# Optimization experiments

Measured on AMD Instinct MI355X. Metric: run time of the kernel, lower is better.

Reference implementation:

```python
import jax, jax.numpy as jnp
import numpy as np

N_NODES = 50000
N_EDGES = 800000
H = 128   # hidden_dim
E = 64    # edge_dim
LN_EPS = 1e-5


def _layer_norm(x, g, b):
    m = jnp.mean(x, axis=-1, keepdims=True)
    v = jnp.mean(jnp.square(x - m), axis=-1, keepdims=True)
    return (x - m) * jax.lax.rsqrt(v + LN_EPS) * g + b


def _gelu(x):
    return jax.nn.gelu(x, approximate=False)  # torch default exact GELU


def setup_inputs() -> dict:
    key = jax.random.key(0)
    ks = jax.random.split(key, 24)

    def lin(k, fin, fout):
        kw, kb = jax.random.split(k)
        s = 1.0 / np.sqrt(fin)
        W = jax.random.uniform(kw, (fin, fout), jnp.float32, -s, s)
        b = jax.random.uniform(kb, (fout,), jnp.float32, -s, s)
        return W, b

    inp = {}
    inp["x"] = jax.random.normal(ks[0], (N_NODES, H), jnp.float32)
    inp["edge_emb"] = jax.random.normal(ks[1], (N_EDGES, E), jnp.float32)
    inp["time_weight"] = jax.random.uniform(ks[2], (N_EDGES, 1), jnp.float32)
    inp["message_node_scale"] = jax.random.uniform(ks[3], (N_NODES, 1), jnp.float32)
    inp["ln1_g"] = jnp.ones((H,), jnp.float32)
    inp["ln1_b"] = jnp.zeros((H,), jnp.float32)
    inp["ln2_g"] = jnp.ones((H,), jnp.float32)
    inp["ln2_b"] = jnp.zeros((H,), jnp.float32)
    inp["selfW"], inp["selfb"] = lin(ks[4], H, H)
    inp["msgW1"], inp["msgb1"] = lin(ks[5], H + E, H)
    inp["msgW2"], inp["msgb2"] = lin(ks[6], H, H)
    inp["gateW1"], inp["gateb1"] = lin(ks[7], 2 * H + E, H)
    inp["gateW2"], inp["gateb2"] = lin(ks[8], H, 1)
    inp["aggW"], inp["aggb"] = lin(ks[9], H, H)
    inp["ffnW1"], inp["ffnb1"] = lin(ks[10], H, 2 * H)
    inp["ffnW2"], inp["ffnb2"] = lin(ks[11], 2 * H, H)
    inp["edge_src"] = jax.random.randint(ks[12], (N_EDGES,), 0, N_NODES, jnp.int32)
    inp["edge_dst"] = jax.random.randint(ks[13], (N_EDGES,), 0, N_NODES, jnp.int32)
    return inp


def reference(x, edge_emb, time_weight, message_node_scale,
              ln1_g, ln1_b, ln2_g, ln2_b,
              selfW, selfb, msgW1, msgb1, msgW2, msgb2,
              gateW1, gateb1, gateW2, gateb2,
              aggW, aggb, ffnW1, ffnb1, ffnW2, ffnb2,
              edge_src, edge_dst):
    n_nodes = x.shape[0]
    n_edges = edge_dst.shape[0]

    h = _layer_norm(x, ln1_g, ln1_b)
    hs = h[edge_src]  # [NE, H]
    hd = h[edge_dst]  # [NE, H]

    msg = _gelu(jnp.concatenate([hs, edge_emb], -1) @ msgW1 + msgb1) @ msgW2 + msgb2
    gate = jax.nn.sigmoid(
        _gelu(jnp.concatenate([hd, hs, edge_emb], -1) @ gateW1 + gateb1) @ gateW2 + gateb2)
    edge_repr = gate * msg
    edge_repr = edge_repr * time_weight
    edge_scale = 0.5 * (message_node_scale[edge_src] + message_node_scale[edge_dst])
    edge_repr = edge_repr * edge_scale

    agg = jax.ops.segment_sum(edge_repr, edge_dst, num_segments=n_nodes)
    deg = jax.ops.segment_sum(jnp.ones((n_edges, 1), x.dtype), edge_dst,
                              num_segments=n_nodes)
    agg = agg / jnp.maximum(deg, 1.0)

    update = (h @ selfW + selfb) + (agg @ aggW + aggb)
    out = x + update  # residual; dropout is identity at inference

    h2 = _layer_norm(out, ln2_g, ln2_b)
    ffn_update = _gelu(h2 @ ffnW1 + ffnb1) @ ffnW2 + ffnb2
    out = out + ffn_update
    return (out, edge_repr)
```

## Files before the change

### kernel.cpp

```cpp
#include <hip/hip_runtime.h>


typedef __attribute__((ext_vector_type(8))) short short8;
typedef __attribute__((ext_vector_type(4))) float f32x4;

#define NN 50000
#define NEDGE 800000

#define MFMA(a, b, c) __builtin_amdgcn_mfma_f32_16x16x32_bf16(a, b, c, 0, 0, 0)

__device__ __forceinline__ unsigned short f2bf(float f) {
  unsigned int u = __float_as_uint(f);
  u += 0x7fffu + ((u >> 16) & 1u);
  return (unsigned short)(u >> 16);
}
__device__ __forceinline__ float bf2f(unsigned short u) {
  return __uint_as_float((unsigned int)u << 16);
}
__device__ __forceinline__ unsigned int cvtpk(float a, float b) {
  unsigned int d;
  asm("v_cvt_pk_bf16_f32 %0, %1, %2" : "=v"(d) : "v"(a), "v"(b));
  return d;
}
__device__ __forceinline__ unsigned short f2bf1(float a) {
  return (unsigned short)cvtpk(a, a);
}
__device__ __forceinline__ float geluf(float x) {
  const float t = x * fmaf(-0.1029437f, x * x, -2.3022211f);
  return x * __builtin_amdgcn_rcpf(1.0f + exp2f(t));
}
__device__ __forceinline__ short8 ld8(const unsigned short* p) {
  return *reinterpret_cast<const short8*>(p);
}
__device__ __forceinline__ int swz256(int row, int byteoff) {
  return row * 256 + (byteoff ^ ((row & 15) << 4));
}
__device__ __forceinline__ int swz128(int row, int byteoff) {
  return row * 128 + (byteoff ^ ((row & 7) << 4));
}

__device__ __forceinline__ void ln_frags(const float* __restrict__ rowp,
                                         const float* __restrict__ g,
                                         const float* __restrict__ b, int koff,
                                         short8 a[4]) {
  f32x4 v[8];
#pragma unroll
  for (int s = 0; s < 4; s++) {
    v[2 * s] = *reinterpret_cast<const f32x4*>(rowp + s * 32 + koff);
    v[2 * s + 1] = *reinterpret_cast<const f32x4*>(rowp + s * 32 + koff + 4);
  }
  float sm = 0.f;
#pragma unroll
  for (int i = 0; i < 8; i++) sm += v[i][0] + v[i][1] + v[i][2] + v[i][3];
  sm += __shfl_xor(sm, 16);
  sm += __shfl_xor(sm, 32);
  const float mean = sm * 0.0078125f;
  float sq = 0.f;
#pragma unroll
  for (int i = 0; i < 8; i++) {
#pragma unroll
    for (int t = 0; t < 4; t++) {
      const float d = v[i][t] - mean;
      sq += d * d;
    }
  }
  sq += __shfl_xor(sq, 16);
  sq += __shfl_xor(sq, 32);
  const float rs = rsqrtf(sq * 0.0078125f + 1e-5f);
#pragma unroll
  for (int s = 0; s < 4; s++) {
    const f32x4 glo = *reinterpret_cast<const f32x4*>(g + s * 32 + koff);
    const f32x4 ghi = *reinterpret_cast<const f32x4*>(g + s * 32 + koff + 4);
    const f32x4 blo = *reinterpret_cast<const f32x4*>(b + s * 32 + koff);
    const f32x4 bhi = *reinterpret_cast<const f32x4*>(b + s * 32 + koff + 4);
    float y[8];
#pragma unroll
    for (int t = 0; t < 4; t++) {
      y[t] = (v[2 * s][t] - mean) * rs * glo[t] + blo[t];
      y[4 + t] = (v[2 * s + 1][t] - mean) * rs * ghi[t] + bhi[t];
    }
    union { unsigned int u[4]; short8 s8; } pk;
    pk.u[0] = cvtpk(y[0], y[1]);
    pk.u[1] = cvtpk(y[2], y[3]);
    pk.u[2] = cvtpk(y[4], y[5]);
    pk.u[3] = cvtpk(y[6], y[7]);
    a[s] = pk.s8;
  }
}

__global__ __launch_bounds__(256) void prep_kernel(
    const float* __restrict__ selfW, const float* __restrict__ msgW1,
    const float* __restrict__ msgW2, const float* __restrict__ gateW1,
    const float* __restrict__ aggW, const float* __restrict__ ffnW1,
    const float* __restrict__ ffnW2, unsigned short* __restrict__ wts,
    int* __restrict__ cnt) {
  const int idx = blockIdx.x * 256 + threadIdx.x;
  if (idx <= NN) cnt[idx] = 0;
  if (idx < 16384) {
    int n = idx >> 7, k = idx & 127;
    wts[idx] = f2bf(selfW[k * 128 + n]);
  } else if (idx < 32768) {
    int l = idx - 16384, n = l >> 7, k = l & 127;
    wts[idx] = f2bf(aggW[k * 128 + n]);
  } else if (idx < 57344) {
    int l = idx - 32768, n = l / 192, k = l - n * 192;
    wts[idx] = f2bf(msgW1[k * 128 + n]);
  } else if (idx < 73728) {
    int l = idx - 57344, n = l >> 7, k = l & 127;
    wts[idx] = f2bf(msgW2[k * 128 + n]);
  } else if (idx < 114688) {
    int l = idx - 73728, n = l / 320, k = l - n * 320;
    wts[idx] = f2bf(gateW1[k * 128 + n]);
  } else if (idx < 147456) {
    int l = idx - 114688, n = l >> 7, k = l & 127;
    wts[idx] = f2bf(ffnW1[k * 256 + n]);
  } else if (idx < 180224) {
    int l = idx - 147456, n = l >> 8, k = l & 255;
    wts[idx] = f2bf(ffnW2[k * 128 + n]);
  }
}

__global__ __launch_bounds__(256) void node_pre_kernel(
    const float* __restrict__ x, const float* __restrict__ ln1g,
    const float* __restrict__ ln1b, const unsigned short* __restrict__ wts,
    unsigned short* __restrict__ pd, unsigned short* __restrict__ psm,
    float* __restrict__ aggf) {
  const int wid = threadIdx.x >> 6, lane = threadIdx.x & 63;
  const int q = lane >> 4, r16 = lane & 15, koff = q * 8;
  const int r0 = blockIdx.x * 64 + wid * 16;
  const int row = min(r0 + r16, NN - 1);
  {
    const int t = blockIdx.x * 256 + threadIdx.x;
    const f32x4 z = (f32x4){0.f, 0.f, 0.f, 0.f};
#pragma unroll
    for (int k = 0; k < 8; k++) {
      const int pos = t + k * 200192;
      if (pos < NN * 32) reinterpret_cast<f32x4*>(aggf)[pos] = z;
    }
  }
  const unsigned short* gateW1T = wts + 73728;
  const unsigned short* msgW1T = wts + 32768;
  short8 a[4];
  ln_frags(x + (size_t)row * 128, ln1g, ln1b, koff, a);
  f32x4 acc[3][8];
#pragma unroll
  for (int t = 0; t < 3; t++)
#pragma unroll
    for (int nt = 0; nt < 8; nt++) acc[t][nt] = (f32x4){0.f, 0.f, 0.f, 0.f};
#pragma unroll
  for (int s = 0; s < 4; s++) {
    const int k0 = s * 32 + koff;
#pragma unroll
    for (int nt = 0; nt < 8; nt++) {
      const int c = nt * 16 + r16;
      acc[0][nt] = MFMA(a[s], ld8(gateW1T + c * 320 + k0), acc[0][nt]);
      acc[1][nt] = MFMA(a[s], ld8(gateW1T + c * 320 + 128 + k0), acc[1][nt]);
      acc[2][nt] = MFMA(a[s], ld8(msgW1T + c * 192 + k0), acc[2][nt]);
    }
  }
#pragma unroll
  for (int j = 0; j < 4; j++) {
    const int gr = r0 + q * 4 + j;
    if (gr < NN) {
#pragma unroll
      for (int nt = 0; nt < 8; nt++) {
        const int c = nt * 16 + r16;
        pd[(size_t)gr * 128 + c] = f2bf(acc[0][nt][j]);
        psm[(size_t)gr * 256 + c] = f2bf(acc[1][nt][j]);
        psm[(size_t)gr * 256 + 128 + c] = f2bf(acc[2][nt][j]);
      }
    }
  }
}

__global__ __launch_bounds__(256) void count_kernel(
    const int* __restrict__ edst, int* __restrict__ cnt) {
  const int e = blockIdx.x * 256 + threadIdx.x;
  atomicAdd(&cnt[edst[e]], 1);
}

__global__ __launch_bounds__(256) void scan_sums_kernel(
    const int* __restrict__ cnt, int* __restrict__ bsum) {
  const int gi = blockIdx.x * 256 + threadIdx.x;
  int v = (gi < NN) ? cnt[gi] : 0;
#pragma unroll
  for (int m = 1; m < 64; m <<= 1) v += __shfl_xor(v, m);
  __shared__ int wsum[4];
  if ((threadIdx.x & 63) == 0) wsum[threadIdx.x >> 6] = v;
  __syncthreads();
  if (threadIdx.x == 0)
    bsum[blockIdx.x] = wsum[0] + wsum[1] + wsum[2] + wsum[3];
}

__global__ __launch_bounds__(256) void scan_offsets_kernel(
    const int* __restrict__ bsum, int* __restrict__ boff, int nb) {
  __shared__ int tmp[256];
  const int tid = threadIdx.x;
  const int v = (tid < nb) ? bsum[tid] : 0;
  tmp[tid] = v;
  __syncthreads();
#pragma unroll
  for (int d = 1; d < 256; d <<= 1) {
    const int t = (tid >= d) ? tmp[tid - d] : 0;
    __syncthreads();
    tmp[tid] += t;
    __syncthreads();
  }
  if (tid < nb) boff[tid] = tmp[tid] - v;
}

__global__ __launch_bounds__(256) void scan_final_kernel(
    const int* __restrict__ cnt, const int* __restrict__ boff,
    int* __restrict__ row_start, int* __restrict__ cursor) {
  const int tid = threadIdx.x, lane = tid & 63, wid = tid >> 6;
  const int gi = blockIdx.x * 256 + tid;
  const int val = (gi < NN) ? cnt[gi] : 0;
  int v = val;
#pragma unroll
  for (int d = 1; d < 64; d <<= 1) {
    const int t = __shfl_up(v, d);
    if (lane >= d) v += t;
  }
  __shared__ int wsum[4];
  if (lane == 63) wsum[wid] = v;
  __syncthreads();
  int woff = 0;
  for (int w = 0; w < wid; ++w) woff += wsum[w];
  const int excl = (v - val) + woff + boff[blockIdx.x];
  if (gi < NN) {
    row_start[gi] = excl;
    cursor[gi] = excl;
  }
  if (gi == NN - 1) row_start[NN] = excl + val;
}

__global__ __launch_bounds__(256) void scatter_kernel(
    const int* __restrict__ esrc, const int* __restrict__ edst,
    const float* __restrict__ tw, const float* __restrict__ mns,
    int* __restrict__ cursor, int4* __restrict__ etab) {
  const int e = blockIdx.x * 256 + threadIdx.x;
  const int si = esrc[e];
  const int di = edst[e];
  const int pos = atomicAdd(&cursor[di], 1);
  const float sc = tw[e] * 0.5f * (mns[si] + mns[di]);
  int4 v;
  v.x = e;
  v.y = si;
  v.z = di;
  v.w = __float_as_int(sc);
  etab[pos] = v;
}

__global__ __launch_bounds__(512, 6) void edge_kernel(
    const float* __restrict__ emb, const int4* __restrict__ etab,
    const unsigned short* __restrict__ pd,
    const unsigned short* __restrict__ psm,
    const unsigned short* __restrict__ wts, const float* __restrict__ msgb1,
    const float* __restrict__ msgb2, const float* __restrict__ gateb1,
    const float* __restrict__ gateW2, const float* __restrict__ gateb2v,
    float* __restrict__ erout, float* __restrict__ aggf) {
  __shared__ __align__(16) char buf[64 * 256 + 64 * 256 + 64 * 128];
  __shared__ float p_s[4][64];
  __shared__ float G_s[64];
  __shared__ float sc_s[64];
  __shared__ int di_s[64], eidx_s[64];

  char* pgp = buf;
  char* pmp = buf + 16384;
  char* embp = buf + 32768;
  float* xbuf = (float*)buf;

  const int tid = threadIdx.x;
  const int lane = tid & 63;
  const int wid = tid >> 6;
  const int q = lane >> 4;
  const int r16 = lane & 15;
  const int koff = q * 8;
  const int mg = wid >> 2;
  const int ng = wid & 3;
  const int e0 = blockIdx.x * 64;

  const unsigned short* gateW1T = wts + 73728;
  const unsigned short* msgW1T = wts + 32768;
  const unsigned short* msgW2T = wts + 57344;

  if (tid < 64) {
    const int4 et = etab[e0 + tid];
    eidx_s[tid] = et.x;
    di_s[tid] = et.z;
    sc_s[tid] = __int_as_float(et.w);
  }

#pragma unroll
  for (int r = 0; r < 2; r++) {
    const int unit = tid + 512 * r;
    const int row = unit >> 4;
    const int c = unit & 15;
    const int4 et = etab[e0 + row];
    const int si = et.y, di = et.z;
    const short8 vd = ld8(pd + (size_t)di * 128 + c * 8);
    const short8 vs = ld8(psm + (size_t)si * 256 + c * 8);
    union { unsigned int u[4]; short8 s; } pk;
#pragma unroll
    for (int h = 0; h < 4; h++) {
      const float f0 =
          bf2f((unsigned short)vd[2 * h]) + bf2f((unsigned short)vs[2 * h]);
      const float f1 = bf2f((unsigned short)vd[2 * h + 1]) +
                       bf2f((unsigned short)vs[2 * h + 1]);
      pk.u[h] = cvtpk(f0, f1);
    }
    *reinterpret_cast<short8*>(pgp + swz256(row, c * 16)) = pk.s;
    *reinterpret_cast<short8*>(pmp + swz256(row, c * 16)) =
        ld8(psm + (size_t)si * 256 + 128 + c * 8);
  }
#pragma unroll
  for (int r = 0; r < 2; r++) {
    const int unit = tid + 512 * r;
    const int row = unit >> 4;
    const int c4 = unit & 15;
    const int e = etab[e0 + row].x;
    const f32x4 v =
        *reinterpret_cast<const f32x4*>(emb + (size_t)e * 64 + c4 * 4);
    uint2 w;
    w.x = cvtpk(v[0], v[1]);
    w.y = cvtpk(v[2], v[3]);
    *reinterpret_cast<uint2*>(embp + swz128(row, c4 * 8)) = w;
  }
  __syncthreads();

  int cc[2];
  float g1[2], w2[2], b1m[2], b2m[2];
#pragma unroll
  for (int i = 0; i < 2; i++) {
    cc[i] = ng * 32 + i * 16 + r16;
    g1[i] = gateb1[cc[i]];
    w2[i] = gateW2[cc[i]];
    b1m[i] = msgb1[cc[i]];
    b2m[i] = msgb2[cc[i]];
  }

  short8 bI[2];
#pragma unroll
  for (int h = 0; h < 8; h++) {
    const int kk = koff + h;
    bI[0][h] = (kk == r16) ? (short)0x3F80 : (short)0;
    bI[1][h] = (kk == r16 + 16) ? (short)0x3F80 : (short)0;
  }

  f32x4 accg[2][2], acc1[2][2];
#pragma unroll
  for (int m = 0; m < 2; m++)
#pragma unroll
    for (int i = 0; i < 2; i++) {
      accg[m][i] = (f32x4){0.f, 0.f, 0.f, 0.f};
      acc1[m][i] = (f32x4){0.f, 0.f, 0.f, 0.f};
    }
#pragma unroll
  for (int s = 0; s < 2; s++) {
    const int k0 = s * 32 + koff;
    short8 a[2];
#pragma unroll
    for (int m = 0; m < 2; m++)
      a[m] = *reinterpret_cast<const short8*>(
          embp + swz128(mg * 32 + m * 16 + r16, k0 * 2));
#pragma unroll
    for (int i = 0; i < 2; i++) {
      const short8 bg = ld8(gateW1T + cc[i] * 320 + 256 + k0);
      const short8 bm = ld8(msgW1T + cc[i] * 192 + 128 + k0);
#pragma unroll
      for (int m = 0; m < 2; m++) {
        accg[m][i] = MFMA(a[m], bg, accg[m][i]);
        acc1[m][i] = MFMA(a[m], bm, acc1[m][i]);
      }
    }
  }

  {
    const int kw = ng * 32 + koff;
#pragma unroll
    for (int m = 0; m < 2; m++) {
      const int row = mg * 32 + m * 16 + r16;
      const short8 apg =
          *reinterpret_cast<const short8*>(pgp + swz256(row, kw * 2));
      const short8 apm =
          *reinterpret_cast<const short8*>(pmp + swz256(row, kw * 2));
#pragma unroll
      for (int i = 0; i < 2; i++) {
        accg[m][i] = MFMA(apg, bI[i], accg[m][i]);
        acc1[m][i] = MFMA(apm, bI[i], acc1[m][i]);
      }
    }
  }

#pragma unroll
  for (int m = 0; m < 2; m++) {
#pragma unroll
    for (int j = 0; j < 4; j++) {
      const int row = mg * 32 + m * 16 + q * 4 + j;
      float v = geluf(accg[m][0][j] + g1[0]) * w2[0] +
                geluf(accg[m][1][j] + g1[1]) * w2[1];
      v += __shfl_xor(v, 1);
      v += __shfl_xor(v, 2);
      v += __shfl_xor(v, 4);
      v += __shfl_xor(v, 8);
      if (r16 == 0) p_s[ng][row] = v;
    }
  }

#pragma unroll
  for (int m = 0; m < 2; m++) {
#pragma unroll
    for (int i = 0; i < 2; i++) {
#pragma unroll
      for (int j = 0; j < 4; j++) {
        const int row = mg * 32 + m * 16 + q * 4 + j;
        *reinterpret_cast<unsigned short*>(pmp + swz256(row, cc[i] * 2)) =
            f2bf1(geluf(acc1[m][i][j] + b1m[i]));
      }
    }
  }
  __syncthreads();

  if (tid < 64) {
    const float p = gateb2v[0] + p_s[0][tid] + p_s[1][tid] + p_s[2][tid] +
                    p_s[3][tid];
    G_s[tid] =
        sc_s[tid] * __builtin_amdgcn_rcpf(1.f + exp2f(-1.4426950f * p));
  }

  f32x4 acc2[2][2];
#pragma unroll
  for (int m = 0; m < 2; m++)
#pragma unroll
    for (int i = 0; i < 2; i++) acc2[m][i] = (f32x4){0.f, 0.f, 0.f, 0.f};
#pragma unroll
  for (int s = 0; s < 4; s++) {
    const int k0 = s * 32 + koff;
    short8 a[2];
#pragma unroll
    for (int m = 0; m < 2; m++)
      a[m] = *reinterpret_cast<const short8*>(
          pmp + swz256(mg * 32 + m * 16 + r16, k0 * 2));
#pragma unroll
    for (int i = 0; i < 2; i++) {
      const short8 b = ld8(msgW2T + cc[i] * 128 + k0);
#pragma unroll
      for (int m = 0; m < 2; m++) acc2[m][i] = MFMA(a[m], b, acc2[m][i]);
    }
  }
  __syncthreads();

#pragma unroll
  for (int m = 0; m < 2; m++)
#pragma unroll
    for (int i = 0; i < 2; i++)
#pragma unroll
      for (int j = 0; j < 4; j++) {
        const int row = mg * 32 + m * 16 + q * 4 + j;
        xbuf[row * 132 + cc[i]] = G_s[row] * (acc2[m][i][j] + b2m[i]);
      }
  __syncthreads();

#pragma unroll
  for (int u = 0; u < 4; u++) {
    const int unit = tid + u * 512;
    const int r = unit >> 5;
    const int f4 = unit & 31;
    const f32x4 val = *reinterpret_cast<const f32x4*>(&xbuf[r * 132 + f4 * 4]);
    *reinterpret_cast<f32x4*>(erout + (size_t)eidx_s[r] * 128 + f4 * 4) = val;
  }

  {
    const int col = tid & 127;
    const int qt = tid >> 7;
    const int rbeg = qt * 16, rend = rbeg + 16;
    float acc = 0.f;
    int prev = di_s[rbeg];
    for (int r = rbeg; r < rend; ++r) {
      const int d = di_s[r];
      if (d != prev) {
        atomicAdd(&aggf[(size_t)prev * 128 + col], acc);
        acc = 0.f;
        prev = d;
      }
      acc += xbuf[r * 132 + col];
    }
    atomicAdd(&aggf[(size_t)prev * 128 + col], acc);
  }
}

__global__ __launch_bounds__(256) void node1_kernel(
    const float* __restrict__ x, const float* __restrict__ ln1g,
    const float* __restrict__ ln1b, const float* __restrict__ aggf,
    const int* __restrict__ row_start, const unsigned short* __restrict__ wts,
    const float* __restrict__ selfb, const float* __restrict__ aggb,
    float* __restrict__ out1) {
  const int wid = threadIdx.x >> 6, lane = threadIdx.x & 63;
  const int q = lane >> 4, r16 = lane & 15, koff = q * 8;
  const int r0 = blockIdx.x * 64 + wid * 16;
  const int row = min(r0 + r16, NN - 1);
  const float inv = __builtin_amdgcn_rcpf(
      fmaxf((float)(row_start[row + 1] - row_start[row]), 1.0f));
  const unsigned short* selfWT = wts;
  const unsigned short* aggWT = wts + 16384;
  short8 a1[4];
  ln_frags(x + (size_t)row * 128, ln1g, ln1b, koff, a1);
  f32x4 acc[8];
#pragma unroll
  for (int nt = 0; nt < 8; nt++) acc[nt] = (f32x4){0.f, 0.f, 0.f, 0.f};
#pragma unroll
  for (int s = 0; s < 4; s++) {
    const int k0 = s * 32 + koff;
    const float* ap = aggf + (size_t)row * 128 + k0;
    const f32x4 f0 = *reinterpret_cast<const f32x4*>(ap);
    const f32x4 f1 = *reinterpret_cast<const f32x4*>(ap + 4);
    union { unsigned int u[4]; short8 s; } pk;
    pk.u[0] = cvtpk(f0[0] * inv, f0[1] * inv);
    pk.u[1] = cvtpk(f0[2] * inv, f0[3] * inv);
    pk.u[2] = cvtpk(f1[0] * inv, f1[1] * inv);
    pk.u[3] = cvtpk(f1[2] * inv, f1[3] * inv);
#pragma unroll
    for (int nt = 0; nt < 8; nt++) {
      acc[nt] = MFMA(a1[s], ld8(selfWT + (nt * 16 + r16) * 128 + k0), acc[nt]);
      acc[nt] = MFMA(pk.s, ld8(aggWT + (nt * 16 + r16) * 128 + k0), acc[nt]);
    }
  }
#pragma unroll
  for (int j = 0; j < 4; j++) {
    const int gr = r0 + q * 4 + j;
    if (gr < NN) {
#pragma unroll
      for (int nt = 0; nt < 8; nt++) {
        const int c = r16 + 16 * nt;
        out1[(size_t)gr * 128 + c] =
            x[(size_t)gr * 128 + c] + acc[nt][j] + selfb[c] + aggb[c];
      }
    }
  }
}

__global__ __launch_bounds__(256) void ffn_kernel(
    const float* __restrict__ out1, const float* __restrict__ ln2g,
    const float* __restrict__ ln2b, const unsigned short* __restrict__ wts,
    const float* __restrict__ b1, const float* __restrict__ b2,
    float* __restrict__ outp) {
  __shared__ unsigned short ts[4][16 * 264];
  const int wid = threadIdx.x >> 6, lane = threadIdx.x & 63;
  const int q = lane >> 4, r16 = lane & 15, koff = q * 8;
  const int r0 = blockIdx.x * 64 + wid * 16;
  const int row = min(r0 + r16, NN - 1);
  const unsigned short* W1T = wts + 114688;
  const unsigned short* W2T = wts + 147456;
  short8 a[4];
  ln_frags(out1 + (size_t)row * 128, ln2g, ln2b, koff, a);
  f32x4 acc1[16];
#pragma unroll
  for (int nt = 0; nt < 16; nt++) acc1[nt] = (f32x4){0.f, 0.f, 0.f, 0.f};
#pragma unroll
  for (int s = 0; s < 4; s++) {
    const int k0 = s * 32 + koff;
#pragma unroll
    for (int nt = 0; nt < 16; nt++)
      acc1[nt] = MFMA(a[s], ld8(W1T + (nt * 16 + r16) * 128 + k0), acc1[nt]);
  }
  unsigned short* tw_ = ts[wid];
#pragma unroll
  for (int nt = 0; nt < 16; nt++) {
    const int c = r16 + 16 * nt;
    const float bb = b1[c];
#pragma unroll
    for (int j = 0; j < 4; j++)
      tw_[(q * 4 + j) * 264 + c] = f2bf1(geluf(acc1[nt][j] + bb));
  }
  __syncthreads();
  f32x4 acc2[8];
#pragma unroll
  for (int nt = 0; nt < 8; nt++) acc2[nt] = (f32x4){0.f, 0.f, 0.f, 0.f};
#pragma unroll
  for (int s = 0; s < 8; s++) {
    const int k0 = s * 32 + koff;
    const short8 av = *reinterpret_cast<const short8*>(tw_ + r16 * 264 + k0);
#pragma unroll
    for (int nt = 0; nt < 8; nt++)
      acc2[nt] = MFMA(av, ld8(W2T + (nt * 16 + r16) * 256 + k0), acc2[nt]);
  }
#pragma unroll
  for (int j = 0; j < 4; j++) {
    const int gr = r0 + q * 4 + j;
    if (gr < NN) {
#pragma unroll
      for (int nt = 0; nt < 8; nt++) {
        const int c = r16 + 16 * nt;
        outp[(size_t)gr * 128 + c] =
            out1[(size_t)gr * 128 + c] + acc2[nt][j] + b2[c];
      }
    }
  }
}

extern "C" void kernel_launch(void* const* d_in, const int* in_sizes, int n_in,
                              void* d_out, int out_size, void* d_ws,
                              size_t ws_size, hipStream_t stream) {
  (void)in_sizes; (void)n_in; (void)out_size; (void)ws_size;
  const float* x = (const float*)d_in[0];
  const float* emb = (const float*)d_in[1];
  const float* tw = (const float*)d_in[2];
  const float* mns = (const float*)d_in[3];
  const float* ln1g = (const float*)d_in[4];
  const float* ln1b = (const float*)d_in[5];
  const float* ln2g = (const float*)d_in[6];
  const float* ln2b = (const float*)d_in[7];
  const float* selfW = (const float*)d_in[8];
  const float* selfb = (const float*)d_in[9];
  const float* msgW1 = (const float*)d_in[10];
  const float* msgb1 = (const float*)d_in[11];
  const float* msgW2 = (const float*)d_in[12];
  const float* msgb2 = (const float*)d_in[13];
  const float* gateW1 = (const float*)d_in[14];
  const float* gateb1 = (const float*)d_in[15];
  const float* gateW2 = (const float*)d_in[16];
  const float* gateb2 = (const float*)d_in[17];
  const float* aggW = (const float*)d_in[18];
  const float* aggb = (const float*)d_in[19];
  const float* ffnW1 = (const float*)d_in[20];
  const float* ffnb1 = (const float*)d_in[21];
  const float* ffnW2 = (const float*)d_in[22];
  const float* ffnb2 = (const float*)d_in[23];
  const int* esrc = (const int*)d_in[24];
  const int* edst = (const int*)d_in[25];

  char* ws = (char*)d_ws;
  unsigned short* pdb = (unsigned short*)(ws);
  unsigned short* psmb = (unsigned short*)(ws + 25600000);
  float* out1 = (float*)(ws + 51200000);
  unsigned short* wts = (unsigned short*)(ws + 76800000);
  int* cnt = (int*)(ws + 77160448);
  int* row_start = (int*)(ws + 77360640);
  int* cursor = (int*)(ws + 77560832);
  int* bsum = (int*)(ws + 77761024);
  int* boff = (int*)(ws + 77762048);
  int4* etab = (int4*)(ws + 77763072);

  float* out_nodes = (float*)d_out;
  float* out_edges = out_nodes + (size_t)NN * 128;
  float* aggf = out_nodes;

  const int NB_SCAN = (NN + 255) / 256;

  prep_kernel<<<704, 256, 0, stream>>>(selfW, msgW1, msgW2, gateW1, aggW,
                                       ffnW1, ffnW2, wts, cnt);
  node_pre_kernel<<<782, 256, 0, stream>>>(x, ln1g, ln1b, wts, pdb, psmb,
                                           aggf);
  count_kernel<<<3125, 256, 0, stream>>>(edst, cnt);
  scan_sums_kernel<<<NB_SCAN, 256, 0, stream>>>(cnt, bsum);
  scan_offsets_kernel<<<1, 256, 0, stream>>>(bsum, boff, NB_SCAN);
  scan_final_kernel<<<NB_SCAN, 256, 0, stream>>>(cnt, boff, row_start, cursor);
  scatter_kernel<<<3125, 256, 0, stream>>>(esrc, edst, tw, mns, cursor, etab);
  edge_kernel<<<12500, 512, 0, stream>>>(emb, etab, pdb, psmb, wts, msgb1,
                                         msgb2, gateb1, gateW2, gateb2,
                                         out_edges, aggf);
  node1_kernel<<<782, 256, 0, stream>>>(x, ln1g, ln1b, aggf, row_start, wts,
                                        selfb, aggb, out1);
  ffn_kernel<<<782, 256, 0, stream>>>(out1, ln2g, ln2b, wts, ffnb1, ffnb2,
                                      out_nodes);
}
```

Before: 648.1 us.

## Fuse node update with FFN, drop scan offsets kernel, gather edge features directly

Merges the node update and FFN kernels so the intermediate node output stays in registers instead of a workspace round trip. The edge kernel now loads the projected src/dst node features straight into MFMA operand registers instead of staging them through LDS, which cuts shared memory use and a staging pass. The separate scan-offsets kernel is removed; each block instead sums the preceding block totals itself. Costs: redundant prefix summation per block, and the gathers are now issued closer to the MFMA chain, with less latency hiding.

After: 616.6 us. -4.9%, faster.

```diff
diff --git a/kernel.cpp b/kernel.cpp
--- a/kernel.cpp
+++ b/kernel.cpp
@@ -192,28 +192,20 @@
     bsum[blockIdx.x] = wsum[0] + wsum[1] + wsum[2] + wsum[3];
 }
 
-__global__ __launch_bounds__(256) void scan_offsets_kernel(
-    const int* __restrict__ bsum, int* __restrict__ boff, int nb) {
-  __shared__ int tmp[256];
-  const int tid = threadIdx.x;
-  const int v = (tid < nb) ? bsum[tid] : 0;
-  tmp[tid] = v;
-  __syncthreads();
-#pragma unroll
-  for (int d = 1; d < 256; d <<= 1) {
-    const int t = (tid >= d) ? tmp[tid - d] : 0;
-    __syncthreads();
-    tmp[tid] += t;
-    __syncthreads();
-  }
-  if (tid < nb) boff[tid] = tmp[tid] - v;
-}
-
 __global__ __launch_bounds__(256) void scan_final_kernel(
-    const int* __restrict__ cnt, const int* __restrict__ boff,
+    const int* __restrict__ cnt, const int* __restrict__ bsum,
     int* __restrict__ row_start, int* __restrict__ cursor) {
   const int tid = threadIdx.x, lane = tid & 63, wid = tid >> 6;
   const int gi = blockIdx.x * 256 + tid;
+  __shared__ int boff_s;
+  __shared__ int wsum[4];
+  if (wid == 0) {
+    int pre = 0;
+    for (int i = lane; i < blockIdx.x; i += 64) pre += bsum[i];
+#pragma unroll
+    for (int m = 32; m >= 1; m >>= 1) pre += __shfl_xor(pre, m);
+    if (lane == 0) boff_s = pre;
+  }
   const int val = (gi < NN) ? cnt[gi] : 0;
   int v = val;
 #pragma unroll
@@ -221,12 +213,11 @@
     const int t = __shfl_up(v, d);
     if (lane >= d) v += t;
   }
-  __shared__ int wsum[4];
   if (lane == 63) wsum[wid] = v;
   __syncthreads();
   int woff = 0;
   for (int w = 0; w < wid; ++w) woff += wsum[w];
-  const int excl = (v - val) + woff + boff[blockIdx.x];
+  const int excl = (v - val) + woff + boff_s;
   if (gi < NN) {
     row_start[gi] = excl;
     cursor[gi] = excl;
@@ -259,15 +250,14 @@
     const float* __restrict__ msgb2, const float* __restrict__ gateb1,
     const float* __restrict__ gateW2, const float* __restrict__ gateb2v,
     float* __restrict__ erout, float* __restrict__ aggf) {
-  __shared__ __align__(16) char buf[64 * 256 + 64 * 256 + 64 * 128];
+  __shared__ __align__(16) char buf[33792];
   __shared__ float p_s[4][64];
   __shared__ float G_s[64];
   __shared__ float sc_s[64];
-  __shared__ int di_s[64], eidx_s[64];
-
-  char* pgp = buf;
-  char* pmp = buf + 16384;
-  char* embp = buf + 32768;
+  __shared__ int di_s[64], si_s[64], eidx_s[64];
+
+  char* t1p = buf;
+  char* embp = buf + 16384;
   float* xbuf = (float*)buf;
 
   const int tid = threadIdx.x;
@@ -287,32 +277,11 @@
   if (tid < 64) {
     const int4 et = etab[e0 + tid];
     eidx_s[tid] = et.x;
+    si_s[tid] = et.y;
     di_s[tid] = et.z;
     sc_s[tid] = __int_as_float(et.w);
   }
 
-#pragma unroll
-  for (int r = 0; r < 2; r++) {
-    const int unit = tid + 512 * r;
-    const int row = unit >> 4;
-    const int c = unit & 15;
-    const int4 et = etab[e0 + row];
-    const int si = et.y, di = et.z;
-    const short8 vd = ld8(pd + (size_t)di * 128 + c * 8);
-    const short8 vs = ld8(psm + (size_t)si * 256 + c * 8);
-    union { unsigned int u[4]; short8 s; } pk;
-#pragma unroll
-    for (int h = 0; h < 4; h++) {
-      const float f0 =
-          bf2f((unsigned short)vd[2 * h]) + bf2f((unsigned short)vs[2 * h]);
-      const float f1 = bf2f((unsigned short)vd[2 * h + 1]) +
-                       bf2f((unsigned short)vs[2 * h + 1]);
-      pk.u[h] = cvtpk(f0, f1);
-    }
-    *reinterpret_cast<short8*>(pgp + swz256(row, c * 16)) = pk.s;
-    *reinterpret_cast<short8*>(pmp + swz256(row, c * 16)) =
-        ld8(psm + (size_t)si * 256 + 128 + c * 8);
-  }
 #pragma unroll
   for (int r = 0; r < 2; r++) {
     const int unit = tid + 512 * r;
@@ -355,6 +324,25 @@
       accg[m][i] = (f32x4){0.f, 0.f, 0.f, 0.f};
       acc1[m][i] = (f32x4){0.f, 0.f, 0.f, 0.f};
     }
+
+  {
+    const int kw = ng * 32 + koff;
+#pragma unroll
+    for (int m = 0; m < 2; m++) {
+      const int row = mg * 32 + m * 16 + r16;
+      const int si = si_s[row], di = di_s[row];
+      const short8 apd = ld8(pd + (size_t)di * 128 + kw);
+      const short8 aps = ld8(psm + (size_t)si * 256 + kw);
+      const short8 apm = ld8(psm + (size_t)si * 256 + 128 + kw);
+#pragma unroll
+      for (int i = 0; i < 2; i++) {
+        accg[m][i] = MFMA(apd, bI[i], accg[m][i]);
+        accg[m][i] = MFMA(aps, bI[i], accg[m][i]);
+        acc1[m][i] = MFMA(apm, bI[i], acc1[m][i]);
+      }
+    }
+  }
+
 #pragma unroll
   for (int s = 0; s < 2; s++) {
     const int k0 = s * 32 + koff;
@@ -371,23 +359,6 @@
       for (int m = 0; m < 2; m++) {
         accg[m][i] = MFMA(a[m], bg, accg[m][i]);
         acc1[m][i] = MFMA(a[m], bm, acc1[m][i]);
-      }
-    }
-  }
-
-  {
-    const int kw = ng * 32 + koff;
-#pragma unroll
-    for (int m = 0; m < 2; m++) {
-      const int row = mg * 32 + m * 16 + r16;
-      const short8 apg =
-          *reinterpret_cast<const short8*>(pgp + swz256(row, kw * 2));
-      const short8 apm =
-          *reinterpret_cast<const short8*>(pmp + swz256(row, kw * 2));
-#pragma unroll
-      for (int i = 0; i < 2; i++) {
-        accg[m][i] = MFMA(apg, bI[i], accg[m][i]);
-        acc1[m][i] = MFMA(apm, bI[i], acc1[m][i]);
       }
     }
   }
@@ -414,7 +385,7 @@
 #pragma unroll
       for (int j = 0; j < 4; j++) {
         const int row = mg * 32 + m * 16 + q * 4 + j;
-        *reinterpret_cast<unsigned short*>(pmp + swz256(row, cc[i] * 2)) =
+        *reinterpret_cast<unsigned short*>(t1p + swz256(row, cc[i] * 2)) =
             f2bf1(geluf(acc1[m][i][j] + b1m[i]));
       }
     }
@@ -440,7 +411,7 @@
 #pragma unroll
     for (int m = 0; m < 2; m++)
       a[m] = *reinterpret_cast<const short8*>(
-          pmp + swz256(mg * 32 + m * 16 + r16, k0 * 2));
+          t1p + swz256(mg * 32 + m * 16 + r16, k0 * 2));
 #pragma unroll
     for (int i = 0; i < 2; i++) {
       const short8 b = ld8(msgW2T + cc[i] * 128 + k0);
@@ -489,12 +460,16 @@
   }
 }
 
-__global__ __launch_bounds__(256) void node1_kernel(
+__global__ __launch_bounds__(256) void node_ffn_kernel(
     const float* __restrict__ x, const float* __restrict__ ln1g,
     const float* __restrict__ ln1b, const float* __restrict__ aggf,
     const int* __restrict__ row_start, const unsigned short* __restrict__ wts,
     const float* __restrict__ selfb, const float* __restrict__ aggb,
-    float* __restrict__ out1) {
+    const float* __restrict__ ln2g, const float* __restrict__ ln2b,
+    const float* __restrict__ fb1, const float* __restrict__ fb2,
+    float* __restrict__ outp) {
+  __shared__ unsigned short h2s[4][16 * 136];
+  __shared__ unsigned short ts[4][16 * 264];
   const int wid = threadIdx.x >> 6, lane = threadIdx.x & 63;
   const int q = lane >> 4, r16 = lane & 15, koff = q * 8;
   const int r0 = blockIdx.x * 64 + wid * 16;
@@ -503,6 +478,9 @@
       fmaxf((float)(row_start[row + 1] - row_start[row]), 1.0f));
   const unsigned short* selfWT = wts;
   const unsigned short* aggWT = wts + 16384;
+  const unsigned short* W1T = wts + 114688;
+  const unsigned short* W2T = wts + 147456;
+
   short8 a1[4];
   ln_frags(x + (size_t)row * 128, ln1g, ln1b, koff, a1);
   f32x4 acc[8];
@@ -525,6 +503,81 @@
       acc[nt] = MFMA(pk.s, ld8(aggWT + (nt * 16 + r16) * 128 + k0), acc[nt]);
     }
   }
+
+  float o[8][4];
+#pragma unroll
+  for (int j = 0; j < 4; j++) {
+    const int gr = min(r0 + q * 4 + j, NN - 1);
+#pragma unroll
+    for (int nt = 0; nt < 8; nt++) {
+      const int c = r16 + 16 * nt;
+      o[nt][j] = x[(size_t)gr * 128 + c] + acc[nt][j] + selfb[c] + aggb[c];
+    }
+  }
+
+#pragma unroll
+  for (int j = 0; j < 4; j++) {
+    float s1 = 0.f;
+#pragma unroll
+    for (int nt = 0; nt < 8; nt++) s1 += o[nt][j];
+    s1 += __shfl_xor(s1, 1);
+    s1 += __shfl_xor(s1, 2);
+    s1 += __shfl_xor(s1, 4);
+    s1 += __shfl_xor(s1, 8);
+    const float mean = s1 * 0.0078125f;
+    float s2 = 0.f;
+#pragma unroll
+    for (int nt = 0; nt < 8; nt++) {
+      const float d = o[nt][j] - mean;
+      s2 += d * d;
+    }
+    s2 += __shfl_xor(s2, 1);
+    s2 += __shfl_xor(s2, 2);
+    s2 += __shfl_xor(s2, 4);
+    s2 += __shfl_xor(s2, 8);
+    const float rs = rsqrtf(s2 * 0.0078125f + 1e-5f);
+#pragma unroll
+    for (int nt = 0; nt < 8; nt++) {
+      const int c = r16 + 16 * nt;
+      h2s[wid][(q * 4 + j) * 136 + c] =
+          f2bf1((o[nt][j] - mean) * rs * ln2g[c] + ln2b[c]);
+    }
+  }
+
+  f32x4 acc1[16];
+#pragma unroll
+  for (int nt = 0; nt < 16; nt++) acc1[nt] = (f32x4){0.f, 0.f, 0.f, 0.f};
+#pragma unroll
+  for (int s = 0; s < 4; s++) {
+    const int k0 = s * 32 + koff;
+    const short8 a =
+        *reinterpret_cast<const short8*>(&h2s[wid][r16 * 136 + k0]);
+#pragma unroll
+    for (int nt = 0; nt < 16; nt++)
+      acc1[nt] = MFMA(a, ld8(W1T + (nt * 16 + r16) * 128 + k0), acc1[nt]);
+  }
+#pragma unroll
+  for (int nt = 0; nt < 16; nt++) {
+    const int c = r16 + 16 * nt;
+    const float bb = fb1[c];
+#pragma unroll
+    for (int j = 0; j < 4; j++)
+      ts[wid][(q * 4 + j) * 264 + c] = f2bf1(geluf(acc1[nt][j] + bb));
+  }
+
+  f32x4 acc2[8];
+#pragma unroll
+  for (int nt = 0; nt < 8; nt++) acc2[nt] = (f32x4){0.f, 0.f, 0.f, 0.f};
+#pragma unroll
+  for (int s = 0; s < 8; s++) {
+    const int k0 = s * 32 + koff;
+    const short8 av =
+        *reinterpret_cast<const short8*>(&ts[wid][r16 * 264 + k0]);
+#pragma unroll
+    for (int nt = 0; nt < 8; nt++)
+      acc2[nt] = MFMA(av, ld8(W2T + (nt * 16 + r16) * 256 + k0), acc2[nt]);
+  }
+
 #pragma unroll
   for (int j = 0; j < 4; j++) {
     const int gr = r0 + q * 4 + j;
@@ -532,67 +585,7 @@
 #pragma unroll
       for (int nt = 0; nt < 8; nt++) {
         const int c = r16 + 16 * nt;
-        out1[(size_t)gr * 128 + c] =
-            x[(size_t)gr * 128 + c] + acc[nt][j] + selfb[c] + aggb[c];
-      }
-    }
-  }
-}
-
-__global__ __launch_bounds__(256) void ffn_kernel(
-    const float* __restrict__ out1, const float* __restrict__ ln2g,
-    const float* __restrict__ ln2b, const unsigned short* __restrict__ wts,
-    const float* __restrict__ b1, const float* __restrict__ b2,
-    float* __restrict__ outp) {
-  __shared__ unsigned short ts[4][16 * 264];
-  const int wid = threadIdx.x >> 6, lane = threadIdx.x & 63;
-  const int q = lane >> 4, r16 = lane & 15, koff = q * 8;
-  const int r0 = blockIdx.x * 64 + wid * 16;
-  const int row = min(r0 + r16, NN - 1);
-  const unsigned short* W1T = wts + 114688;
-  const unsigned short* W2T = wts + 147456;
-  short8 a[4];
-  ln_frags(out1 + (size_t)row * 128, ln2g, ln2b, koff, a);
-  f32x4 acc1[16];
-#pragma unroll
-  for (int nt = 0; nt < 16; nt++) acc1[nt] = (f32x4){0.f, 0.f, 0.f, 0.f};
-#pragma unroll
-  for (int s = 0; s < 4; s++) {
-    const int k0 = s * 32 + koff;
-#pragma unroll
-    for (int nt = 0; nt < 16; nt++)
-      acc1[nt] = MFMA(a[s], ld8(W1T + (nt * 16 + r16) * 128 + k0), acc1[nt]);
-  }
-  unsigned short* tw_ = ts[wid];
-#pragma unroll
-  for (int nt = 0; nt < 16; nt++) {
-    const int c = r16 + 16 * nt;
-    const float bb = b1[c];
-#pragma unroll
-    for (int j = 0; j < 4; j++)
-      tw_[(q * 4 + j) * 264 + c] = f2bf1(geluf(acc1[nt][j] + bb));
-  }
-  __syncthreads();
-  f32x4 acc2[8];
-#pragma unroll
-  for (int nt = 0; nt < 8; nt++) acc2[nt] = (f32x4){0.f, 0.f, 0.f, 0.f};
-#pragma unroll
-  for (int s = 0; s < 8; s++) {
-    const int k0 = s * 32 + koff;
-    const short8 av = *reinterpret_cast<const short8*>(tw_ + r16 * 264 + k0);
-#pragma unroll
-    for (int nt = 0; nt < 8; nt++)
-      acc2[nt] = MFMA(av, ld8(W2T + (nt * 16 + r16) * 256 + k0), acc2[nt]);
-  }
-#pragma unroll
-  for (int j = 0; j < 4; j++) {
-    const int gr = r0 + q * 4 + j;
-    if (gr < NN) {
-#pragma unroll
-      for (int nt = 0; nt < 8; nt++) {
-        const int c = r16 + 16 * nt;
-        outp[(size_t)gr * 128 + c] =
-            out1[(size_t)gr * 128 + c] + acc2[nt][j] + b2[c];
+        outp[(size_t)gr * 128 + c] = o[nt][j] + acc2[nt][j] + fb2[c];
       }
     }
   }
@@ -632,13 +625,11 @@
   char* ws = (char*)d_ws;
   unsigned short* pdb = (unsigned short*)(ws);
   unsigned short* psmb = (unsigned short*)(ws + 25600000);
-  float* out1 = (float*)(ws + 51200000);
   unsigned short* wts = (unsigned short*)(ws + 76800000);
   int* cnt = (int*)(ws + 77160448);
   int* row_start = (int*)(ws + 77360640);
   int* cursor = (int*)(ws + 77560832);
   int* bsum = (int*)(ws + 77761024);
-  int* boff = (int*)(ws + 77762048);
   int4* etab = (int4*)(ws + 77763072);
 
   float* out_nodes = (float*)d_out;
@@ -653,14 +644,12 @@
                                            aggf);
   count_kernel<<<3125, 256, 0, stream>>>(edst, cnt);
   scan_sums_kernel<<<NB_SCAN, 256, 0, stream>>>(cnt, bsum);
-  scan_offsets_kernel<<<1, 256, 0, stream>>>(bsum, boff, NB_SCAN);
-  scan_final_kernel<<<NB_SCAN, 256, 0, stream>>>(cnt, boff, row_start, cursor);
+  scan_final_kernel<<<NB_SCAN, 256, 0, stream>>>(cnt, bsum, row_start, cursor);
   scatter_kernel<<<3125, 256, 0, stream>>>(esrc, edst, tw, mns, cursor, etab);
   edge_kernel<<<12500, 512, 0, stream>>>(emb, etab, pdb, psmb, wts, msgb1,
                                          msgb2, gateb1, gateW2, gateb2,
                                          out_edges, aggf);
-  node1_kernel<<<782, 256, 0, stream>>>(x, ln1g, ln1b, aggf, row_start, wts,
-                                        selfb, aggb, out1);
-  ffn_kernel<<<782, 256, 0, stream>>>(out1, ln2g, ln2b, wts, ffnb1, ffnb2,
-                                      out_nodes);
-}
+  node_ffn_kernel<<<782, 256, 0, stream>>>(x, ln1g, ln1b, aggf, row_start,
+                                           wts, selfb, aggb, ln2g, ln2b,
+                                           ffnb1, ffnb2, out_nodes);
+}
```
